# Performance work log

Measured on AMD Instinct MI355X. Metric: run time of the kernel, lower is better.

Reference implementation:

```python
import jax, jax.numpy as jnp
import numpy as np

N = 100_000
E = 1_600_000
HID = 128
HEADS = 4
HD = HID // HEADS
EPS = 1e-5


def _ln(x, g, b):
    m = jnp.mean(x, axis=-1, keepdims=True)
    v = jnp.mean((x - m) ** 2, axis=-1, keepdims=True)
    return (x - m) * jax.lax.rsqrt(v + EPS) * g + b


def setup_inputs() -> dict:
    key = jax.random.key(0)
    ks = jax.random.split(key, 12)
    xav = lambda k, i, o: jax.random.uniform(k, (i, o), jnp.float32, -1.0, 1.0) * (0.1 * np.sqrt(6.0 / (i + o)))
    return {
        "h": jax.random.normal(ks[0], (N, HID), jnp.float32),
        "src": jax.random.randint(ks[1], (E,), 0, N, jnp.int32),
        "dst": jax.random.randint(ks[2], (E,), 0, N, jnp.int32),
        "Wq": xav(ks[3], HID, HID), "bq": jnp.zeros((HID,), jnp.float32),
        "Wk": xav(ks[4], HID, HID), "bk": jnp.zeros((HID,), jnp.float32),
        "Wv": xav(ks[5], HID, HID), "bv": jnp.zeros((HID,), jnp.float32),
        "Wo": xav(ks[6], HID, HID), "bo": jnp.zeros((HID,), jnp.float32),
        "W1": xav(ks[7], HID, 2 * HID), "b1": jnp.zeros((2 * HID,), jnp.float32),
        "W2": xav(ks[8], 2 * HID, HID), "b2": jnp.zeros((HID,), jnp.float32),
        "g1": jnp.ones((HID,), jnp.float32), "be1": jnp.zeros((HID,), jnp.float32),
        "g2": jnp.ones((HID,), jnp.float32), "be2": jnp.zeros((HID,), jnp.float32),
    }


def reference(h, src, dst, Wq, bq, Wk, bk, Wv, bv, Wo, bo, W1, b1, W2, b2, g1, be1, g2, be2):
    scale = HD ** -0.5
    h_norm = _ln(h, g1, be1)
    Q = (h_norm @ Wq + bq).reshape(N, HEADS, HD)
    K = (h_norm @ Wk + bk).reshape(N, HEADS, HD)
    V = (h_norm @ Wv + bv).reshape(N, HEADS, HD)

    # edge scores: q[dst] . k[src]  -> [E, HEADS]
    scores = jnp.sum(Q[dst] * K[src], axis=-1) * scale

    # edge softmax per destination node (segment softmax)
    smax = jax.ops.segment_max(scores, dst, num_segments=N)  # [N, HEADS]
    ex = jnp.exp(scores - smax[dst])
    denom = jax.ops.segment_sum(ex, dst, num_segments=N)
    alpha = ex / denom[dst]  # [E, HEADS]

    # weighted aggregation: sum over incoming edges of alpha * v[src]
    msgs = alpha[:, :, None] * V[src]  # [E, HEADS, HD]
    h_new = jax.ops.segment_sum(msgs, dst, num_segments=N).reshape(N, HID)

    h_attn = h_new @ Wo + bo
    h = h + h_attn  # dropout = identity (eval)
    h2 = _ln(h, g2, be2)
    ffn = jax.nn.relu(h2 @ W1 + b1) @ W2 + b2
    return h + ffn
```

## Files before the change

kernel.cpp:

```cpp
#include <hip/hip_runtime.h>
#include <math.h>

#define HIDN 128
#define EPS 1e-5f
#define ATT_SCALE 0.17677669529663687f

typedef unsigned int  u32;
typedef unsigned short u16;
typedef __attribute__((ext_vector_type(8))) short bf16x8;
typedef __attribute__((ext_vector_type(4))) float f32x4;
typedef __attribute__((ext_vector_type(2))) _Float16 h16x2;

__device__ __forceinline__ u16 f2b(float x) {
    u32 u = __float_as_uint(x);
    u += 0x7FFFu + ((u >> 16) & 1u);
    return (u16)(u >> 16);
}
__device__ __forceinline__ float b2f(u16 x) { return __uint_as_float(((u32)x) << 16); }
__device__ __forceinline__ u16 f2h(float x) {
    _Float16 h = (_Float16)x;
    u16 r; __builtin_memcpy(&r, &h, 2); return r;
}
__device__ __forceinline__ h16x2 u2h(u32 a) { h16x2 r; __builtin_memcpy(&r, &a, 4); return r; }

__device__ __forceinline__ float dot2f(u32 a, u32 b, float c) {
    h16x2 ah = u2h(a), bh = u2h(b);
#if __has_builtin(__builtin_amdgcn_fdot2)
    return __builtin_amdgcn_fdot2(ah, bh, c, false);
#else
    return c + (float)ah.x * (float)bh.x + (float)ah.y * (float)bh.y;
#endif
}

#define MFMA(a, b, c) __builtin_amdgcn_mfma_f32_16x16x32_bf16((a), (b), (c), 0, 0, 0)

__device__ __forceinline__ int swz(int row, int kpos, int rowstride) {
    return row * rowstride + ((((kpos >> 3) ^ (row & 7)) << 3) | (kpos & 7));
}

__global__ __launch_bounds__(256) void k_pack_all(
    const float* __restrict__ Wq, const float* __restrict__ Wk, const float* __restrict__ Wv,
    const float* __restrict__ Wo, const float* __restrict__ W1, const float* __restrict__ W2,
    u16* __restrict__ out)
{
    int idx = blockIdx.x * 256 + threadIdx.x;
    const float* W; int K, N, base, local;
    if      (idx <  2048) { W = Wq; K = 128; N = 128; base = 0;     local = idx; }
    else if (idx <  4096) { W = Wk; K = 128; N = 128; base = 16384; local = idx - 2048; }
    else if (idx <  6144) { W = Wv; K = 128; N = 128; base = 32768; local = idx - 4096; }
    else if (idx <  8192) { W = Wo; K = 128; N = 128; base = 49152; local = idx - 6144; }
    else if (idx < 12288) { W = W1; K = 128; N = 256; base = 65536; local = idx - 8192; }
    else if (idx < 16384) { W = W2; K = 256; N = 128; base = 98304; local = idx - 12288; }
    else return;
    const int KC = K >> 5;
    const int l  = local & 63;
    const int tc = local >> 6;
    const int c  = tc % KC;
    const int t  = tc / KC;
    const int col = l & 15, hg = l >> 4;
    const int kbase = c * 32 + hg * 8;
    u16 v[8];
    #pragma unroll
    for (int j = 0; j < 8; ++j) v[j] = f2b(W[(size_t)(kbase + j) * N + t * 16 + col]);
    uint4 o;
    o.x = (u32)v[0] | ((u32)v[1] << 16);
    o.y = (u32)v[2] | ((u32)v[3] << 16);
    o.z = (u32)v[4] | ((u32)v[5] << 16);
    o.w = (u32)v[6] | ((u32)v[7] << 16);
    *(uint4*)&out[base + local * 8] = o;
}

__global__ __launch_bounds__(256) void k_qkv(
    const float* __restrict__ h, const float* __restrict__ g1, const float* __restrict__ be1,
    const u16* __restrict__ Bq, const u16* __restrict__ Bk, const u16* __restrict__ Bv,
    const float* __restrict__ bq, const float* __restrict__ bk, const float* __restrict__ bv,
    u16* __restrict__ Qh, u16* __restrict__ KVb, int M)
{
    __shared__ u16 smem[4][4096];
    const int wid = threadIdx.x >> 6;
    const int l   = threadIdx.x & 63;
    int slab = blockIdx.x * 4 + wid;
    const bool valid = (slab * 16) < M;
    if (!valid) slab = 0;
    const int r0  = slab * 16;
    const int col = l & 15, hg = l >> 4;
    u16* ws = smem[wid];

    float av[4][8];
    const float* hr = h + (size_t)(r0 + col) * 128 + hg * 8;
    #pragma unroll
    for (int c = 0; c < 4; ++c) {
        float4 p0 = *(const float4*)&hr[c * 32];
        float4 p1 = *(const float4*)&hr[c * 32 + 4];
        av[c][0] = p0.x; av[c][1] = p0.y; av[c][2] = p0.z; av[c][3] = p0.w;
        av[c][4] = p1.x; av[c][5] = p1.y; av[c][6] = p1.z; av[c][7] = p1.w;
    }
    float s = 0.f, q2 = 0.f;
    #pragma unroll
    for (int c = 0; c < 4; ++c)
        #pragma unroll
        for (int j = 0; j < 8; ++j) { float v = av[c][j]; s += v; q2 += v * v; }
    s  += __shfl_xor(s, 16);  s  += __shfl_xor(s, 32);
    q2 += __shfl_xor(q2, 16); q2 += __shfl_xor(q2, 32);
    float mean = s * (1.f / 128.f);
    float var  = q2 * (1.f / 128.f) - mean * mean;
    float rs   = rsqrtf(var + EPS);

    bf16x8 af[4];
    #pragma unroll
    for (int c = 0; c < 4; ++c) {
        u32 w[4];
        #pragma unroll
        for (int jj = 0; jj < 4; ++jj) {
            int k0 = c * 32 + hg * 8 + 2 * jj;
            float v0 = (av[c][2 * jj]     - mean) * rs * g1[k0]     + be1[k0];
            float v1 = (av[c][2 * jj + 1] - mean) * rs * g1[k0 + 1] + be1[k0 + 1];
            w[jj] = (u32)f2b(v0) | ((u32)f2b(v1) << 16);
        }
        uint4 uu = make_uint4(w[0], w[1], w[2], w[3]);
        af[c] = *(bf16x8*)&uu;
    }

    #pragma unroll
    for (int t = 0; t < 8; ++t) {
        float bb = bq[t * 16 + col];
        f32x4 c = {bb, bb, bb, bb};
        const u16* bp = Bq + t * 2048 + l * 8;
        c = MFMA(af[0], *(const bf16x8*)(bp),        c);
        c = MFMA(af[1], *(const bf16x8*)(bp + 512),  c);
        c = MFMA(af[2], *(const bf16x8*)(bp + 1024), c);
        c = MFMA(af[3], *(const bf16x8*)(bp + 1536), c);
        #pragma unroll
        for (int r = 0; r < 4; ++r)
            ws[swz(hg * 4 + r, t * 16 + col, 256)] = f2h(c[r]);
    }
    __syncthreads();
    if (valid) {
        #pragma unroll
        for (int i = 0; i < 4; ++i) {
            int row = i * 4 + (l >> 4);
            int cg  = l & 15;
            bf16x8 vv = *(const bf16x8*)&ws[swz(row, cg * 8, 256)];
            *(bf16x8*)&Qh[(size_t)(r0 + row) * 128 + cg * 8] = vv;
        }
    }
    __syncthreads();

    #pragma unroll
    for (int t = 0; t < 8; ++t) {
        float bb = bk[t * 16 + col];
        f32x4 c = {bb, bb, bb, bb};
        const u16* bp = Bk + t * 2048 + l * 8;
        c = MFMA(af[0], *(const bf16x8*)(bp),        c);
        c = MFMA(af[1], *(const bf16x8*)(bp + 512),  c);
        c = MFMA(af[2], *(const bf16x8*)(bp + 1024), c);
        c = MFMA(af[3], *(const bf16x8*)(bp + 1536), c);
        int cc = t * 16 + col;
        int kp = ((cc >> 1) << 2) | (cc & 1);
        #pragma unroll
        for (int r = 0; r < 4; ++r)
            ws[swz(hg * 4 + r, kp, 256)] = f2h(c[r]);
    }
    #pragma unroll
    for (int t = 0; t < 8; ++t) {
        float bb = bv[t * 16 + col];
        f32x4 c = {bb, bb, bb, bb};
        const u16* bp = Bv + t * 2048 + l * 8;
        c = MFMA(af[0], *(const bf16x8*)(bp),        c);
        c = MFMA(af[1], *(const bf16x8*)(bp + 512),  c);
        c = MFMA(af[2], *(const bf16x8*)(bp + 1024), c);
        c = MFMA(af[3], *(const bf16x8*)(bp + 1536), c);
        int cc = t * 16 + col;
        int kp = ((cc >> 1) << 2) | 2 | (cc & 1);
        #pragma unroll
        for (int r = 0; r < 4; ++r)
            ws[swz(hg * 4 + r, kp, 256)] = f2h(c[r]);
    }
    __syncthreads();
    if (valid) {
        #pragma unroll
        for (int i = 0; i < 8; ++i) {
            int row = i * 2 + (l >> 5);
            int g   = l & 31;
            bf16x8 vv = *(const bf16x8*)&ws[swz(row, g * 8, 256)];
            *(bf16x8*)&KVb[(size_t)(r0 + row) * 256 + g * 8] = vv;
        }
    }
}

#define BSH 8
#define CHUNK 4096

__global__ __launch_bounds__(256) void k_bcount(
    const int* __restrict__ dst, int* __restrict__ bcnt, int e)
{
    __shared__ int hist[512];
    const int tid = threadIdx.x;
    hist[tid] = 0; hist[tid + 256] = 0;
    __syncthreads();
    const int i0 = blockIdx.x * CHUNK;
    #pragma unroll
    for (int t = 0; t < CHUNK / 256; ++t) {
        int i = i0 + t * 256 + tid;
        if (i < e) atomicAdd(&hist[dst[i] >> BSH], 1);
    }
    __syncthreads();
    for (int j = tid; j < 512; j += 256) {
        int c = hist[j];
        if (c) atomicAdd(&bcnt[j], c);
    }
}

__global__ __launch_bounds__(512) void k_bscan(
    const int* __restrict__ bcnt, int* __restrict__ bbase, int* __restrict__ bcur, int nbuck)
{
    __shared__ int ts[512];
    const int tid = threadIdx.x;
    int v = (tid < nbuck) ? bcnt[tid] : 0;
    ts[tid] = v;
    __syncthreads();
    for (int off = 1; off < 512; off <<= 1) {
        int x = (tid >= off) ? ts[tid - off] : 0;
        __syncthreads();
        ts[tid] += x;
        __syncthreads();
    }
    int ex = ts[tid] - v;
    if (tid <= nbuck) bbase[tid] = ex;
    if (tid < nbuck)  bcur[tid]  = ex;
}

__global__ __launch_bounds__(256) void k_bscatter(
    const int* __restrict__ src, const int* __restrict__ dst,
    int* __restrict__ bcur, int2* __restrict__ ebuf, int e)
{
    __shared__ int hist[512];
    __shared__ int lbase[512];
    __shared__ int lrun[512];
    const int tid = threadIdx.x;
    hist[tid] = 0; hist[tid + 256] = 0;
    __syncthreads();
    const int i0 = blockIdx.x * CHUNK;
    #pragma unroll
    for (int t = 0; t < CHUNK / 256; ++t) {
        int i = i0 + t * 256 + tid;
        if (i < e) atomicAdd(&hist[dst[i] >> BSH], 1);
    }
    __syncthreads();
    for (int j = tid; j < 512; j += 256) {
        int c = hist[j];
        lrun[j] = 0;
        if (c) lbase[j] = atomicAdd(&bcur[j], c);
    }
    __syncthreads();
    #pragma unroll
    for (int t = 0; t < CHUNK / 256; ++t) {
        int i = i0 + t * 256 + tid;
        if (i < e) {
            int d = dst[i];
            int b = d >> BSH;
            int r = atomicAdd(&lrun[b], 1);
            ebuf[lbase[b] + r] = make_int2(src[i], d);
        }
    }
}

__global__ __launch_bounds__(256) void k_bbuild(
    const int2* __restrict__ ebuf, const int* __restrict__ bbase,
    int* __restrict__ cnt, int* __restrict__ offs, int* __restrict__ csrc, int n)
{
    __shared__ int ncnt[256];
    __shared__ int ts[256];
    __shared__ int nrun[256];
    const int tid = threadIdx.x;
    const int b = blockIdx.x;
    const int node0 = b << BSH;
    const int nn = min(256, n - node0);
    const int s = bbase[b];
    const int epb = bbase[b + 1] - s;

    ncnt[tid] = 0;
    __syncthreads();
    for (int i = tid; i < epb; i += 256)
        atomicAdd(&ncnt[ebuf[s + i].y & 255], 1);
    __syncthreads();
    int v = ncnt[tid];
    ts[tid] = v;
    __syncthreads();
    for (int off = 1; off < 256; off <<= 1) {
        int x = (tid >= off) ? ts[tid - off] : 0;
        __syncthreads();
        ts[tid] += x;
        __syncthreads();
    }
    int ex = ts[tid] - v;
    if (tid < nn) { cnt[node0 + tid] = v; offs[node0 + tid] = s + ex; }
    nrun[tid] = 0;
    __syncthreads();
    ncnt[tid] = ex;
    __syncthreads();
    for (int i = tid; i < epb; i += 256) {
        int2 p = ebuf[s + i];
        int d = p.y & 255;
        int r = atomicAdd(&nrun[d], 1);
        csrc[s + ncnt[d] + r] = p.x;
    }
}

__global__ __launch_bounds__(256) void k_edge(
    const u16* __restrict__ Qh, const u16* __restrict__ KVb,
    const int* __restrict__ offs, const int* __restrict__ cnt, const int* __restrict__ csrc,
    u16* __restrict__ hnew, int n)
{
    const int wid  = threadIdx.x >> 6;
    const int l    = threadIdx.x & 63;
    const int node = blockIdx.x * 4 + wid;
    if (node >= n) return;
    const int start = offs[node];
    const int deg   = cnt[node];
    const int w    = l & 15;
    const int slot = l >> 4;

    const uint4 q = *(const uint4*)&Qh[(size_t)node * 128 + w * 8];

    h16x2 o0 = {0, 0}, o1 = {0, 0}, o2 = {0, 0}, o3 = {0, 0};
    float denom = 0.f;

    for (int base = 0; base < deg; base += 64) {
        int m = deg - base; if (m > 64) m = 64;
        int myidx = 0;
        if (l < m) myidx = csrc[start + base + l];
        for (int j = 0; j < m; j += 4) {
            int eloc = j + slot;
            int s = __shfl(myidx, eloc & 63);
            const u16* kvr = KVb + (size_t)s * 256 + w * 16;
            uint4 kv0 = *(const uint4*)(kvr);
            uint4 kv1 = *(const uint4*)(kvr + 8);
            float p = dot2f(kv0.x, q.x, 0.f);
            p = dot2f(kv0.z, q.y, p);
            p = dot2f(kv1.x, q.z, p);
            p = dot2f(kv1.z, q.w, p);
            p += __shfl_xor(p, 1);
            p += __shfl_xor(p, 2);
            float al = __expf(p * ATT_SCALE);
            al = (eloc < m) ? al : 0.f;
            denom += al;
            h16x2 a2; a2.x = (_Float16)al; a2.y = a2.x;
            o0 += a2 * u2h(kv0.y);
            o1 += a2 * u2h(kv0.w);
            o2 += a2 * u2h(kv1.y);
            o3 += a2 * u2h(kv1.w);
        }
    }

    float of[8];
    of[0] = (float)o0.x; of[1] = (float)o0.y; of[2] = (float)o1.x; of[3] = (float)o1.y;
    of[4] = (float)o2.x; of[5] = (float)o2.y; of[6] = (float)o3.x; of[7] = (float)o3.y;
    #pragma unroll
    for (int msk = 16; msk <= 32; msk <<= 1) {
        #pragma unroll
        for (int i = 0; i < 8; ++i) of[i] += __shfl_xor(of[i], msk);
        denom += __shfl_xor(denom, msk);
    }
    float inv = (deg > 0) ? (1.f / denom) : 0.f;
    if (slot == 0) {
        u32 wrd[4];
        #pragma unroll
        for (int i = 0; i < 4; ++i)
            wrd[i] = (u32)f2b(of[2 * i] * inv) | ((u32)f2b(of[2 * i + 1] * inv) << 16);
        uint4 uu = make_uint4(wrd[0], wrd[1], wrd[2], wrd[3]);
        *(uint4*)&hnew[(size_t)node * 128 + w * 8] = uu;
    }
}

__global__ __launch_bounds__(256) void k_attnout(
    const u16* __restrict__ hnew, const u16* __restrict__ Bo, const float* __restrict__ bo,
    const float* __restrict__ h, const float* __restrict__ g2, const float* __restrict__ be2,
    float* __restrict__ h1, u16* __restrict__ h2, int M)
{
    const int slab = blockIdx.x * 4 + (threadIdx.x >> 6);
    const int l = threadIdx.x & 63;
    const int r0 = slab * 16;
    if (r0 >= M) return;
    const int col = l & 15, hg = l >> 4;
    const u16* ar = hnew + (size_t)(r0 + col) * 128 + hg * 8;
    bf16x8 a0 = *(const bf16x8*)(ar);
    bf16x8 a1 = *(const bf16x8*)(ar + 32);
    bf16x8 a2 = *(const bf16x8*)(ar + 64);
    bf16x8 a3 = *(const bf16x8*)(ar + 96);
    f32x4 acc[8];
    #pragma unroll
    for (int t = 0; t < 8; ++t) {
        float bb = bo[t * 16 + col];
        f32x4 c = {bb, bb, bb, bb};
        const u16* bp = Bo + t * 2048 + l * 8;
        c = MFMA(a0, *(const bf16x8*)(bp),        c);
        c = MFMA(a1, *(const bf16x8*)(bp + 512),  c);
        c = MFMA(a2, *(const bf16x8*)(bp + 1024), c);
        c = MFMA(a3, *(const bf16x8*)(bp + 1536), c);
        acc[t] = c;
    }
    float s[4] = {0, 0, 0, 0}, s2[4] = {0, 0, 0, 0};
    #pragma unroll
    for (int t = 0; t < 8; ++t) {
        #pragma unroll
        for (int r = 0; r < 4; ++r) {
            float x = acc[t][r] + h[(size_t)(r0 + hg * 4 + r) * 128 + t * 16 + col];
            acc[t][r] = x;
            s[r] += x; s2[r] += x * x;
        }
    }
    float mean[4], rs[4];
    #pragma unroll
    for (int r = 0; r < 4; ++r) {
        float a = s[r], b = s2[r];
        a += __shfl_xor(a, 1); b += __shfl_xor(b, 1);
        a += __shfl_xor(a, 2); b += __shfl_xor(b, 2);
        a += __shfl_xor(a, 4); b += __shfl_xor(b, 4);
        a += __shfl_xor(a, 8); b += __shfl_xor(b, 8);
        mean[r] = a * (1.f / 128.f);
        float var = b * (1.f / 128.f) - mean[r] * mean[r];
        rs[r] = rsqrtf(var + EPS);
    }
    #pragma unroll
    for (int t = 0; t < 8; ++t) {
        float g  = g2[t * 16 + col];
        float be = be2[t * 16 + col];
        #pragma unroll
        for (int r = 0; r < 4; ++r) {
            size_t idx = (size_t)(r0 + hg * 4 + r) * 128 + t * 16 + col;
            float x = acc[t][r];
            h1[idx] = x;
            h2[idx] = f2b((x - mean[r]) * rs[r] * g + be);
        }
    }
}

__global__ __launch_bounds__(256) void k_ffn1(
    const u16* __restrict__ h2, const u16* __restrict__ B1, const float* __restrict__ b1,
    u16* __restrict__ tb, int M)
{
    const int slab = blockIdx.x * 4 + (threadIdx.x >> 6);
    const int l = threadIdx.x & 63;
    const int r0 = slab * 16;
    if (r0 >= M) return;
    const int col = l & 15, hg = l >> 4;
    const u16* ar = h2 + (size_t)(r0 + col) * 128 + hg * 8;
    bf16x8 a0 = *(const bf16x8*)(ar);
    bf16x8 a1 = *(const bf16x8*)(ar + 32);
    bf16x8 a2 = *(const bf16x8*)(ar + 64);
    bf16x8 a3 = *(const bf16x8*)(ar + 96);
    #pragma unroll
    for (int t = 0; t < 16; ++t) {
        float bb = b1[t * 16 + col];
        f32x4 c = {bb, bb, bb, bb};
        const u16* bp = B1 + t * 2048 + l * 8;
        c = MFMA(a0, *(const bf16x8*)(bp),        c);
        c = MFMA(a1, *(const bf16x8*)(bp + 512),  c);
        c = MFMA(a2, *(const bf16x8*)(bp + 1024), c);
        c = MFMA(a3, *(const bf16x8*)(bp + 1536), c);
        #pragma unroll
        for (int r = 0; r < 4; ++r)
            tb[(size_t)(r0 + hg * 4 + r) * 256 + t * 16 + col] = f2b(fmaxf(c[r], 0.f));
    }
}

__global__ __launch_bounds__(256) void k_ffn2(
    const u16* __restrict__ tb, const u16* __restrict__ B2, const float* __restrict__ b2,
    const float* __restrict__ h1, float* __restrict__ out, int M)
{
    const int slab = blockIdx.x * 4 + (threadIdx.x >> 6);
    const int l = threadIdx.x & 63;
    const int r0 = slab * 16;
    if (r0 >= M) return;
    const int col = l & 15, hg = l >> 4;
    const u16* ar = tb + (size_t)(r0 + col) * 256 + hg * 8;
    bf16x8 a[8];
    #pragma unroll
    for (int i = 0; i < 8; ++i) a[i] = *(const bf16x8*)(ar + i * 32);
    #pragma unroll
    for (int t = 0; t < 8; ++t) {
        float bb = b2[t * 16 + col];
        f32x4 c = {bb, bb, bb, bb};
        const u16* bp = B2 + t * 4096 + l * 8;
        #pragma unroll
        for (int kc = 0; kc < 8; ++kc)
            c = MFMA(a[kc], *(const bf16x8*)(bp + kc * 512), c);
        #pragma unroll
        for (int r = 0; r < 4; ++r) {
            size_t idx = (size_t)(r0 + hg * 4 + r) * 128 + t * 16 + col;
            out[idx] = c[r] + h1[idx];
        }
    }
}

extern "C" void kernel_launch(void* const* d_in, const int* in_sizes, int n_in,
                              void* d_out, int out_size, void* d_ws, size_t ws_size,
                              hipStream_t stream)
{
    const float* h   = (const float*)d_in[0];
    const int*   src = (const int*)  d_in[1];
    const int*   dst = (const int*)  d_in[2];
    const float* Wq  = (const float*)d_in[3];
    const float* bq  = (const float*)d_in[4];
    const float* Wk  = (const float*)d_in[5];
    const float* bk  = (const float*)d_in[6];
    const float* Wv  = (const float*)d_in[7];
    const float* bv  = (const float*)d_in[8];
    const float* Wo  = (const float*)d_in[9];
    const float* bo  = (const float*)d_in[10];
    const float* W1  = (const float*)d_in[11];
    const float* b1  = (const float*)d_in[12];
    const float* W2  = (const float*)d_in[13];
    const float* b2  = (const float*)d_in[14];
    const float* g1  = (const float*)d_in[15];
    const float* be1 = (const float*)d_in[16];
    const float* g2  = (const float*)d_in[17];
    const float* be2 = (const float*)d_in[18];

    const int n = in_sizes[0] / HIDN;
    const int e = in_sizes[1];
    float* out = (float*)d_out;

    const int nbuck = (n + 255) >> BSH;

    char* p = (char*)d_ws;
    int* csrc  = (int*)p;              p += (size_t)e * 4;
    int* cnt   = (int*)p;              p += (size_t)n * 4;
    int* offs  = (int*)p;              p += (size_t)n * 4;
    int* bcnt  = (int*)p;              p += 512 * 4;
    int* bbase = (int*)p;              p += 512 * 4;
    int* bcur  = (int*)p;              p += 512 * 4;
    u16* wpack = (u16*)p;              p += 131072 * 2;
    u16* KVb  = (u16*)p;               p += (size_t)n * 256 * 2;
    u16* Qh   = (u16*)p;               p += (size_t)n * 128 * 2;
    u16* hnew = (u16*)p;               p += (size_t)n * 128 * 2;
    float* h1 = (float*)p;             p += (size_t)n * 128 * 4;
    u16* h2 = Qh;
    u16* tb = KVb;
    int2* ebuf = (int2*)h1;

    u16* Wq_p = wpack;
    u16* Wk_p = wpack + 16384;
    u16* Wv_p = wpack + 32768;
    u16* Wo_p = wpack + 49152;
    u16* W1_p = wpack + 65536;
    u16* W2_p = wpack + 98304;

    const int nslab = (n + 15) / 16;
    const int gemm_blocks = (nslab + 3) / 4;
    const int echunks = (e + CHUNK - 1) / CHUNK;

    hipMemsetAsync(bcnt, 0, 512 * sizeof(int), stream);

    k_bcount  <<<echunks, 256, 0, stream>>>(dst, bcnt, e);
    k_bscan   <<<1, 512, 0, stream>>>(bcnt, bbase, bcur, nbuck);
    k_bscatter<<<echunks, 256, 0, stream>>>(src, dst, bcur, ebuf, e);
    k_bbuild  <<<nbuck, 256, 0, stream>>>(ebuf, bbase, cnt, offs, csrc, n);

    k_pack_all<<<64, 256, 0, stream>>>(Wq, Wk, Wv, Wo, W1, W2, wpack);

    k_qkv <<<gemm_blocks, 256, 0, stream>>>(h, g1, be1, Wq_p, Wk_p, Wv_p,
                                            bq, bk, bv, Qh, KVb, n);

    k_edge<<<(n + 3) / 4, 256, 0, stream>>>(Qh, KVb, offs, cnt, csrc, hnew, n);

    k_attnout<<<gemm_blocks, 256, 0, stream>>>(hnew, Wo_p, bo, h, g2, be2, h1, h2, n);

    k_ffn1<<<gemm_blocks, 256, 0, stream>>>(h2, W1_p, b1, tb, n);

    k_ffn2<<<gemm_blocks, 256, 0, stream>>>(tb, W2_p, b2, h1, out, n);
}
```

Baseline: 464.6 us.

## Store K/V in FP8 to halve edge gather bytes

The QKV kernel now packs K and V into FP8 (e4m3 via hardware cvt_pk when available), shrinking each node's interleaved KV row from 512 to 256 bytes. The edge kernel gathers one 16-byte chunk per lane instead of two and accumulates scores and outputs in fp32 after unpacking. This targets the random-gather bandwidth of the edge aggregation, which is the dominant memory cost. It trades away K/V precision, adds unpack instructions, and moves the FFN temp buffer to its own workspace allocation because KVb can no longer alias it.

```diff
diff --git a/kernel.cpp b/kernel.cpp
--- a/kernel.cpp
+++ b/kernel.cpp
@@ -9,6 +9,7 @@
 typedef unsigned short u16;
 typedef __attribute__((ext_vector_type(8))) short bf16x8;
 typedef __attribute__((ext_vector_type(4))) float f32x4;
+typedef __attribute__((ext_vector_type(2))) float f32x2;
 typedef __attribute__((ext_vector_type(2))) _Float16 h16x2;
 
 __device__ __forceinline__ u16 f2b(float x) {
@@ -23,12 +24,36 @@
 }
 __device__ __forceinline__ h16x2 u2h(u32 a) { h16x2 r; __builtin_memcpy(&r, &a, 4); return r; }
 
-__device__ __forceinline__ float dot2f(u32 a, u32 b, float c) {
-    h16x2 ah = u2h(a), bh = u2h(b);
-#if __has_builtin(__builtin_amdgcn_fdot2)
-    return __builtin_amdgcn_fdot2(ah, bh, c, false);
+#if __has_builtin(__builtin_amdgcn_cvt_pk_f32_fp8) && __has_builtin(__builtin_amdgcn_cvt_pk_fp8_f32)
+#define HW_FP8 1
 #else
-    return c + (float)ah.x * (float)bh.x + (float)ah.y * (float)bh.y;
+#define HW_FP8 0
+#endif
+
+__device__ __forceinline__ u32 pk_fp8(float a, float b) {
+#if HW_FP8
+    return ((u32)__builtin_amdgcn_cvt_pk_fp8_f32(a, b, 0, false)) & 0xFFFFu;
+#else
+    u16 ha = f2h(a), hb = f2h(b);
+    u32 b0 = (((u32)ha) + 0x80u + ((ha >> 8) & 1u)) >> 8;
+    u32 b1 = (((u32)hb) + 0x80u + ((hb >> 8) & 1u)) >> 8;
+    return (b0 & 0xFFu) | ((b1 & 0xFFu) << 8);
+#endif
+}
+__device__ __forceinline__ f32x2 unpk_fp8_lo(u32 v) {
+#if HW_FP8
+    return __builtin_amdgcn_cvt_pk_f32_fp8(v, false);
+#else
+    h16x2 hh = u2h(((v & 0xFFu) << 8) | ((v & 0xFF00u) << 16));
+    f32x2 r; r.x = (float)hh.x; r.y = (float)hh.y; return r;
+#endif
+}
+__device__ __forceinline__ f32x2 unpk_fp8_hi(u32 v) {
+#if HW_FP8
+    return __builtin_amdgcn_cvt_pk_f32_fp8(v, true);
+#else
+    h16x2 hh = u2h(((v >> 16) & 0xFFu) << 8 | ((v >> 24) & 0xFFu) << 24);
+    f32x2 r; r.x = (float)hh.x; r.y = (float)hh.y; return r;
 #endif
 }
 
@@ -76,7 +101,7 @@
     const float* __restrict__ bq, const float* __restrict__ bk, const float* __restrict__ bv,
     u16* __restrict__ Qh, u16* __restrict__ KVb, int M)
 {
-    __shared__ u16 smem[4][4096];
+    __shared__ u16 smem[4][2048];
     const int wid = threadIdx.x >> 6;
     const int l   = threadIdx.x & 63;
     int slab = blockIdx.x * 4 + wid;
@@ -132,7 +157,7 @@
         c = MFMA(af[3], *(const bf16x8*)(bp + 1536), c);
         #pragma unroll
         for (int r = 0; r < 4; ++r)
-            ws[swz(hg * 4 + r, t * 16 + col, 256)] = f2h(c[r]);
+            ws[swz(hg * 4 + r, t * 16 + col, 128)] = f2h(c[r]);
     }
     __syncthreads();
     if (valid) {
@@ -140,7 +165,7 @@
         for (int i = 0; i < 4; ++i) {
             int row = i * 4 + (l >> 4);
             int cg  = l & 15;
-            bf16x8 vv = *(const bf16x8*)&ws[swz(row, cg * 8, 256)];
+            bf16x8 vv = *(const bf16x8*)&ws[swz(row, cg * 8, 128)];
             *(bf16x8*)&Qh[(size_t)(r0 + row) * 128 + cg * 8] = vv;
         }
     }
@@ -156,10 +181,13 @@
         c = MFMA(af[2], *(const bf16x8*)(bp + 1024), c);
         c = MFMA(af[3], *(const bf16x8*)(bp + 1536), c);
         int cc = t * 16 + col;
-        int kp = ((cc >> 1) << 2) | (cc & 1);
-        #pragma unroll
-        for (int r = 0; r < 4; ++r)
-            ws[swz(hg * 4 + r, kp, 256)] = f2h(c[r]);
+        int ki = ((cc >> 3) << 3) | ((cc & 7) >> 1);
+        #pragma unroll
+        for (int r = 0; r < 4; ++r) {
+            float other = __shfl_xor(c[r], 1);
+            if ((col & 1) == 0)
+                ws[swz(hg * 4 + r, ki, 128)] = (u16)pk_fp8(c[r], other);
+        }
     }
     #pragma unroll
     for (int t = 0; t < 8; ++t) {
@@ -171,19 +199,22 @@
         c = MFMA(af[2], *(const bf16x8*)(bp + 1024), c);
         c = MFMA(af[3], *(const bf16x8*)(bp + 1536), c);
         int cc = t * 16 + col;
-        int kp = ((cc >> 1) << 2) | 2 | (cc & 1);
-        #pragma unroll
-        for (int r = 0; r < 4; ++r)
-            ws[swz(hg * 4 + r, kp, 256)] = f2h(c[r]);
+        int vi = (((cc >> 3) << 3) | ((cc & 7) >> 1)) + 4;
+        #pragma unroll
+        for (int r = 0; r < 4; ++r) {
+            float other = __shfl_xor(c[r], 1);
+            if ((col & 1) == 0)
+                ws[swz(hg * 4 + r, vi, 128)] = (u16)pk_fp8(c[r], other);
+        }
     }
     __syncthreads();
     if (valid) {
         #pragma unroll
-        for (int i = 0; i < 8; ++i) {
-            int row = i * 2 + (l >> 5);
-            int g   = l & 31;
-            bf16x8 vv = *(const bf16x8*)&ws[swz(row, g * 8, 256)];
-            *(bf16x8*)&KVb[(size_t)(r0 + row) * 256 + g * 8] = vv;
+        for (int i = 0; i < 4; ++i) {
+            int row = i * 4 + (l >> 4);
+            int cg  = l & 15;
+            bf16x8 vv = *(const bf16x8*)&ws[swz(row, cg * 8, 128)];
+            *(bf16x8*)&KVb[(size_t)(r0 + row) * 128 + cg * 8] = vv;
         }
     }
 }
@@ -322,8 +353,14 @@
     const int slot = l >> 4;
 
     const uint4 q = *(const uint4*)&Qh[(size_t)node * 128 + w * 8];
-
-    h16x2 o0 = {0, 0}, o1 = {0, 0}, o2 = {0, 0}, o3 = {0, 0};
+    float qf[8];
+    { h16x2 t;
+      t = u2h(q.x); qf[0] = (float)t.x; qf[1] = (float)t.y;
+      t = u2h(q.y); qf[2] = (float)t.x; qf[3] = (float)t.y;
+      t = u2h(q.z); qf[4] = (float)t.x; qf[5] = (float)t.y;
+      t = u2h(q.w); qf[6] = (float)t.x; qf[7] = (float)t.y; }
+
+    float of[8] = {0, 0, 0, 0, 0, 0, 0, 0};
     float denom = 0.f;
 
     for (int base = 0; base < deg; base += 64) {
@@ -333,29 +370,36 @@
         for (int j = 0; j < m; j += 4) {
             int eloc = j + slot;
             int s = __shfl(myidx, eloc & 63);
-            const u16* kvr = KVb + (size_t)s * 256 + w * 16;
-            uint4 kv0 = *(const uint4*)(kvr);
-            uint4 kv1 = *(const uint4*)(kvr + 8);
-            float p = dot2f(kv0.x, q.x, 0.f);
-            p = dot2f(kv0.z, q.y, p);
-            p = dot2f(kv1.x, q.z, p);
-            p = dot2f(kv1.z, q.w, p);
+            const uint4 kv = *(const uint4*)&KVb[(size_t)s * 128 + w * 8];
+            f32x2 k01 = unpk_fp8_lo(kv.x), k23 = unpk_fp8_hi(kv.x);
+            f32x2 k45 = unpk_fp8_lo(kv.y), k67 = unpk_fp8_hi(kv.y);
+            float p;
+            p = qf[0] * k01.x;
+            p = fmaf(qf[1], k01.y, p);
+            p = fmaf(qf[2], k23.x, p);
+            p = fmaf(qf[3], k23.y, p);
+            p = fmaf(qf[4], k45.x, p);
+            p = fmaf(qf[5], k45.y, p);
+            p = fmaf(qf[6], k67.x, p);
+            p = fmaf(qf[7], k67.y, p);
             p += __shfl_xor(p, 1);
             p += __shfl_xor(p, 2);
             float al = __expf(p * ATT_SCALE);
             al = (eloc < m) ? al : 0.f;
             denom += al;
-            h16x2 a2; a2.x = (_Float16)al; a2.y = a2.x;
-            o0 += a2 * u2h(kv0.y);
-            o1 += a2 * u2h(kv0.w);
-            o2 += a2 * u2h(kv1.y);
-            o3 += a2 * u2h(kv1.w);
-        }
-    }
-
-    float of[8];
-    of[0] = (float)o0.x; of[1] = (float)o0.y; of[2] = (float)o1.x; of[3] = (float)o1.y;
-    of[4] = (float)o2.x; of[5] = (float)o2.y; of[6] = (float)o3.x; of[7] = (float)o3.y;
+            f32x2 v01 = unpk_fp8_lo(kv.z), v23 = unpk_fp8_hi(kv.z);
+            f32x2 v45 = unpk_fp8_lo(kv.w), v67 = unpk_fp8_hi(kv.w);
+            of[0] = fmaf(al, v01.x, of[0]);
+            of[1] = fmaf(al, v01.y, of[1]);
+            of[2] = fmaf(al, v23.x, of[2]);
+            of[3] = fmaf(al, v23.y, of[3]);
+            of[4] = fmaf(al, v45.x, of[4]);
+            of[5] = fmaf(al, v45.y, of[5]);
+            of[6] = fmaf(al, v67.x, of[6]);
+            of[7] = fmaf(al, v67.y, of[7]);
+        }
+    }
+
     #pragma unroll
     for (int msk = 16; msk <= 32; msk <<= 1) {
         #pragma unroll
@@ -532,12 +576,12 @@
     int* bbase = (int*)p;              p += 512 * 4;
     int* bcur  = (int*)p;              p += 512 * 4;
     u16* wpack = (u16*)p;              p += 131072 * 2;
-    u16* KVb  = (u16*)p;               p += (size_t)n * 256 * 2;
+    u16* KVb  = (u16*)p;               p += (size_t)n * 128 * 2;
     u16* Qh   = (u16*)p;               p += (size_t)n * 128 * 2;
     u16* hnew = (u16*)p;               p += (size_t)n * 128 * 2;
     float* h1 = (float*)p;             p += (size_t)n * 128 * 4;
+    u16* tb   = (u16*)p;               p += (size_t)n * 256 * 2;
     u16* h2 = Qh;
-    u16* tb = KVb;
     int2* ebuf = (int2*)h1;
 
     u16* Wq_p = wpack;
```

New measurement: 408.5 us. -12.1%, faster.
